# Performance work log

Hardware: AMD Instinct MI355X
Metric: run time of the kernel (lower is better)

Reference implementation:

```python
import jax, jax.numpy as jnp
import numpy as np

FOCAL_ALPHA = 0.25
FOCAL_GAMMA = 2.0
W_FOCAL = 1.0
W_DICE = 1.0
COST_MASK = 1.0
COST_DICE = 1.0
COST_CLASS = 0.0
CLS_W_MATCHED = 2.0
CLS_W_NOOBJ = 0.1


def hungarian(cost):
    """Exact Hungarian (shortest augmenting path). cost: [n, m] numpy, n <= m.
    Returns ans[i] = column assigned to row i."""
    cost = np.asarray(cost, dtype=np.float64)
    n, m = cost.shape
    assert n <= m
    INF = 1e18
    u = np.zeros(n + 1)
    v = np.zeros(m + 1)
    p = np.zeros(m + 1, dtype=np.int64)   # p[j] = row (1-indexed) matched to col j
    way = np.zeros(m + 1, dtype=np.int64)
    for i in range(1, n + 1):
        p[0] = i
        j0 = 0
        minv = np.full(m + 1, INF)
        used = np.zeros(m + 1, dtype=bool)
        while True:
            used[j0] = True
            i0 = p[j0]
            cur = cost[i0 - 1, :] - u[i0] - v[1:]
            upd = (~used[1:]) & (cur < minv[1:])
            minv[1:][upd] = cur[upd]
            way[1:][upd] = j0
            free = ~used[1:]
            j1 = int(np.argmin(np.where(free, minv[1:], INF))) + 1
            delta = minv[j1]
            u[p[used]] += delta
            v[used] -= delta
            minv[1:][free] -= delta
            j0 = j1
            if p[j0] == 0:
                break
        while j0:
            j1 = way[j0]
            p[j0] = p[j1]
            j0 = j1
    ans = np.zeros(n, dtype=np.int64)
    for j in range(1, m + 1):
        if p[j] > 0:
            ans[p[j] - 1] = j - 1
    return ans


def _focal_terms(logits):
    # sigmoid focal loss split into positive/negative per-point terms
    p = jax.nn.sigmoid(logits)
    pos = FOCAL_ALPHA * (1.0 - p) ** FOCAL_GAMMA * jax.nn.softplus(-logits)
    neg = (1.0 - FOCAL_ALPHA) * p ** FOCAL_GAMMA * jax.nn.softplus(logits)
    return pos, neg


def _inst_class_first(labels, seg, num_inst, C):
    # class of each instance = class of its FIRST point (reverse scatter so
    # earlier occurrences overwrite later ones), clamped to [0, C-1]
    inst_class = jnp.zeros((num_inst,), jnp.int32).at[labels[::-1]].set(seg[::-1])
    return jnp.clip(inst_class, 0, C - 1)


def _match_cost(pm, logits, tgt, inst_class):
    # pm [Q,N] mask logits, tgt [I,N] binary target masks
    N = pm.shape[1]
    pos, neg = _focal_terms(pm)
    c_focal = (pos @ tgt.T + neg @ (1.0 - tgt).T) / N            # [Q,I]
    p = jax.nn.sigmoid(pm)
    num = 2.0 * (p @ tgt.T)
    den = p.sum(1, keepdims=True) + tgt.sum(1)[None, :]
    c_dice = 1.0 - (num + 1.0) / (den + 1.0)                     # [Q,I]
    prob = jax.nn.softmax(logits, axis=-1)
    c_class = -prob[:, inst_class]                               # [Q,I]
    return COST_MASK * c_focal + COST_DICE * c_dice + COST_CLASS * c_class


def _batch_loss(pm, logits, labels, seg, num_inst, idx_q):
    Q, N = pm.shape
    C = logits.shape[1] - 1
    tgt = (labels[None, :] == jnp.arange(num_inst)[:, None]).astype(pm.dtype)  # [I,N]
    pm_m = pm[idx_q]                                                           # [I,N]
    # focal loss over matched (mask, target-mask) pairs
    pos, neg = _focal_terms(pm_m)
    focal = jnp.mean(pos * tgt + neg * (1.0 - tgt))
    # dice loss
    p = jax.nn.sigmoid(pm_m)
    num = 2.0 * jnp.sum(p * tgt, axis=1)
    den = jnp.sum(p, axis=1) + jnp.sum(tgt, axis=1)
    dice = jnp.mean(1.0 - (num + 1.0) / (den + 1.0))
    # classification: matched queries -> instance class, unmatched -> no-object (C)
    inst_class = _inst_class_first(labels, seg, num_inst, C)
    logp = jax.nn.log_softmax(logits, axis=-1)                 # [Q,C+1]
    ce_matched = -jnp.mean(logp[idx_q, inst_class])
    unmatched = jnp.ones((Q,), bool).at[idx_q].set(False)
    n_un = jnp.sum(unmatched)
    ce_noobj = -jnp.sum(jnp.where(unmatched, logp[:, C], 0.0)) / jnp.maximum(n_un, 1)
    cls = CLS_W_MATCHED * ce_matched + CLS_W_NOOBJ * ce_noobj
    return W_FOCAL * focal + W_DICE * dice + cls


def setup_inputs() -> dict:
    key = jax.random.key(0)
    k1, k2, k3, k4 = jax.random.split(key, 4)
    B, Q, N, I, C1 = 2, 100, 200000, 64, 6
    pred_masks = jax.random.normal(k1, (B, Q, N), dtype=jnp.float32)
    pred_logits = jax.random.normal(k2, (B, Q, C1), dtype=jnp.float32)
    labels = jax.random.randint(k3, (B, N), 0, I).astype(jnp.int32)
    # guarantee every instance id appears at least once
    labels = labels.at[:, :I].set(jnp.arange(I, dtype=jnp.int32)[None, :])
    seg = jax.random.randint(k4, (B, N), 0, C1 - 1).astype(jnp.int32)
    return {"pred_masks": pred_masks, "pred_logits": pred_logits,
            "labels": labels, "seg": seg, "num_instances": I}


def reference(pred_masks, pred_logits, labels, seg, num_instances):
    B = pred_masks.shape[0]
    C = pred_logits.shape[2] - 1
    losses = []
    for b in range(B):  # small fixed batch of events with ragged semantics
        pm, lg, lb, sg = pred_masks[b], pred_logits[b], labels[b], seg[b]
        tgt = (lb[None, :] == jnp.arange(num_instances)[:, None]).astype(pm.dtype)
        inst_class = _inst_class_first(lb, sg, num_instances, C)
        cost = _match_cost(pm, lg, tgt, inst_class)              # [Q,I]
        idx_q = jnp.asarray(hungarian(np.asarray(jax.lax.stop_gradient(cost)).T),
                            dtype=jnp.int32)                     # [I]
        losses.append(_batch_loss(pm, lg, lb, sg, num_instances, idx_q))
    return jnp.mean(jnp.stack(losses))
```

## Files before the change

kernel.cpp:

```cpp
#include <hip/hip_runtime.h>
#include <cstdint>
#include <cstddef>

constexpr int kB  = 2;
constexpr int kQ  = 100;
constexpr int kN  = 200000;
constexpr int kI  = 64;
constexpr int kC1 = 6;
constexpr int kQP = 128;

__global__ void prep_kernel(const int* __restrict__ labels,
                            int* __restrict__ cnt, int* __restrict__ firstIdx) {
  const int b = blockIdx.y;
  const int tid = threadIdx.x;
  __shared__ int lcnt[kI], lmin[kI];
  if (tid < kI) { lcnt[tid] = 0; lmin[tid] = 0x7FFFFFFF; }
  __syncthreads();
  for (int n = blockIdx.x * blockDim.x + tid; n < kN; n += gridDim.x * blockDim.x) {
    int l = labels[(size_t)b * kN + n] & (kI - 1);
    atomicAdd(&lcnt[l], 1);
    atomicMin(&lmin[l], n);
  }
  __syncthreads();
  if (tid < kI) {
    if (lcnt[tid]) atomicAdd(&cnt[b * kI + tid], lcnt[tid]);
    atomicMin(&firstIdx[b * kI + tid], lmin[tid]);
  }
}

__global__ __launch_bounds__(1024) void bucket_kernel(
    const float* __restrict__ pm, const int* __restrict__ labels,
    const int* __restrict__ cnt,
    float* __restrict__ fS, float* __restrict__ pS,
    float* __restrict__ negTot, float* __restrict__ pTot,
    float* __restrict__ costT) {
  const int q = blockIdx.x, b = blockIdx.y;
  const int tid = threadIdx.x;
  const int w = tid >> 6;
  constexpr float kScale = 16384.0f;
  constexpr double kInv  = 1.0 / 16384.0;

  __shared__ unsigned long long lS[16][kI];
  ((unsigned long long*)lS)[tid] = 0ull;
  __syncthreads();

  const float4* row4 = (const float4*)(pm + ((size_t)(b * kQ + q)) * kN);
  const int4*   lab4 = (const int4*)(labels + (size_t)b * kN);
  float negAcc = 0.f;
  constexpr int NV4 = kN / 4;

  for (int it = tid; it < NV4; it += 1024) {
    float4 xv = row4[it];
    int4   lv = lab4[it];
#define PROC(x_, l_) do {                                   \
      float x = (x_); int l = (l_) & (kI - 1);              \
      float xc = fminf(fmaxf(x, -60.f), 60.f);              \
      float t  = __expf(-xc);                               \
      float r  = 1.0f / (1.0f + t);         \
      float L  = __logf(1.0f + t);        \
      float omp = t * r;                         \
      float pos = 0.25f * omp * omp * L;                    \
      float neg = 0.75f * r * r * (L + x);                  \
      int fi = __float2int_rn((pos - neg) * kScale);        \
      int pi = __float2int_rn(r * kScale);                  \
      unsigned long long pk =                               \
        (unsigned long long)(((long long)fi) << 32) +       \
        (unsigned long long)(unsigned int)pi;               \
      atomicAdd(&lS[w][l], pk);                             \
      negAcc += neg;                                        \
    } while (0)
    PROC(xv.x, lv.x); PROC(xv.y, lv.y); PROC(xv.z, lv.z); PROC(xv.w, lv.w);
#undef PROC
  }
  __syncthreads();

  __shared__ float ffS[kI], fpS[kI];
  if (tid < kI) {
    long long fsum = 0, psum = 0;
    for (int ww = 0; ww < 16; ++ww) {
      unsigned long long s = lS[ww][tid];
      fsum += (int)(s >> 32);
      psum += (long long)(s & 0xFFFFFFFFull);
    }
    ffS[tid] = (float)((double)fsum * kInv);
    fpS[tid] = (float)((double)psum * kInv);
  }
  for (int off = 32; off; off >>= 1) negAcc += __shfl_down(negAcc, off);
  __shared__ float wsum[16];
  if ((tid & 63) == 0) wsum[w] = negAcc;
  __syncthreads();
  __shared__ float s_negTot, s_pTot;
  if (tid == 0) {
    float s = 0.f;
    for (int ww = 0; ww < 16; ++ww) s += wsum[ww];
    s_negTot = s;
  }
  if (tid < kI) {
    float vv = fpS[tid];
    for (int off = 32; off; off >>= 1) vv += __shfl_down(vv, off);
    if (tid == 0) s_pTot = vv;
  }
  __syncthreads();

  if (tid < kI) {
    float f = ffS[tid], pp = fpS[tid];
    int bq = b * kQ + q;
    fS[(size_t)bq * kI + tid] = f;
    pS[(size_t)bq * kI + tid] = pp;
    float cf = (f + s_negTot) * (1.0f / kN);
    float cd = 1.0f - (2.0f * pp + 1.0f) / (s_pTot + (float)cnt[b * kI + tid] + 1.0f);
    costT[(size_t)(b * kI + tid) * kQ + q] = cf + cd;
    if (tid == 0) { negTot[bq] = s_negTot; pTot[bq] = s_pTot; }
  }
}

template<int CTRL>
__device__ __forceinline__ int dpp_mov(int x) {
  return __builtin_amdgcn_update_dpp(x, x, CTRL, 0xF, 0xF, false);
}
template<int CTRL>
__device__ __forceinline__ float dpp_minf(float a) {
  int o = dpp_mov<CTRL>(__float_as_int(a));
  return fminf(a, __int_as_float(o));
}
__device__ __forceinline__ double rl64(double x, int l) {
  int lo = __builtin_amdgcn_readlane(__double2loint(x), l);
  int hi = __builtin_amdgcn_readlane(__double2hiint(x), l);
  return __hiloint2double(hi, lo);
}
__device__ __forceinline__ float rlf(float x, int l) {
  return __int_as_float(__builtin_amdgcn_readlane(__float_as_int(x), l));
}
__device__ __forceinline__ float packF(float v, int cid) {
  int bb = __float_as_int(v);
  bb = (bb & ~0x7F) | cid;
  return __int_as_float(bb);
}
__device__ __forceinline__ float maskF(float v) {
  return __int_as_float(__float_as_int(v) & ~0x7F);
}
__device__ __forceinline__ void comb2f(float& m1, float& m2, float o1, float o2) {
  float lo = fminf(m1, o1);
  float hi = fmaxf(m1, o1);
  m2 = fminf(hi, fminf(m2, o2));
  m1 = lo;
}
template<int CTRL>
__device__ __forceinline__ void dpp_comb2f(float& m1, float& m2) {
  float o1 = __int_as_float(dpp_mov<CTRL>(__float_as_int(m1)));
  float o2 = __int_as_float(dpp_mov<CTRL>(__float_as_int(m2)));
  comb2f(m1, m2, o1, o2);
}

__global__ void hungarian_kernel(const float* __restrict__ costT,
                                 int* __restrict__ idx_q) {
  const int b = blockIdx.x;
  const int lane = threadIdx.x;
  __shared__ float costL[kI * kQP];
  for (int t = lane; t < kI * kQP; t += 64) {
    int row = t >> 7, col = t & (kQP - 1);
    costL[t] = (col < kQ) ? costT[(size_t)b * kI * kQ + row * kQ + col] : 1e30f;
  }
  __syncthreads();

  const double INF = 1e18;
  double v0 = 0.0, v1 = 0.0;
  int p0 = 0, p1 = 0;

  double m = INF; int jm = 0;
  for (int k = 0; k < kQ; ++k) {
    double c = (double)costL[lane * kQP + k];
    if (c < m) { m = c; jm = k; }
  }
  double u_r = m;
  unsigned long long rowM = 0ull;
  for (int r = 0; r < kI; ++r) {
    int jmr = __builtin_amdgcn_readlane(jm, r);
    int curp = (jmr < 64) ? __builtin_amdgcn_readlane(p0, jmr)
                          : __builtin_amdgcn_readlane(p1, jmr - 64);
    if (curp == 0) {
      bool m0 = (jmr < 64) && (lane == jmr);
      bool m1b = (jmr >= 64) && (lane == jmr - 64);
      p0 = m0 ? r + 1 : p0;
      p1 = m1b ? r + 1 : p1;
      rowM |= 1ull << r;
    }
  }

  unsigned long long pool = ~rowM;
  unsigned long long leftover = 0ull;
  for (int pass = 0; pass < 2; ++pass) {
    unsigned long long next = 0ull;
    unsigned long long cur = pool;
    while (cur) {
      int i = __builtin_ctzll(cur) + 1;
      cur &= cur - 1;
      const float* crow = &costL[(i - 1) * kQP];
      double e0 = (double)crow[lane] - v0;
      double e1 = (double)crow[lane + 64] - v1;
      float pf0 = packF((float)e0, lane);
      float pf1 = packF((float)e1, lane + 64);
      float m1 = fminf(pf0, pf1), m2 = fmaxf(pf0, pf1);
      dpp_comb2f<0xB1>(m1, m2);
      dpp_comb2f<0x4E>(m1, m2);
      dpp_comb2f<0x141>(m1, m2);
      dpp_comb2f<0x140>(m1, m2);
      float a1 = rlf(m1, 0),  a2 = rlf(m2, 0);
      { float b1 = rlf(m1, 16), b2 = rlf(m2, 16); comb2f(a1, a2, b1, b2); }
      { float b1 = rlf(m1, 32), b2 = rlf(m2, 32); comb2f(a1, a2, b1, b2); }
      { float b1 = rlf(m1, 48), b2 = rlf(m2, 48); comb2f(a1, a2, b1, b2); }
      int cid1 = __builtin_amdgcn_readfirstlane(__float_as_int(a1) & 0x7F);
      int cid2 = __builtin_amdgcn_readfirstlane(__float_as_int(a2) & 0x7F);
      int L1 = cid1 & 63; bool sW = cid1 >= 64;
      int L2 = cid2 & 63; bool sW2 = cid2 >= 64;
      double min1 = sW  ? rl64(e1, L1) : rl64(e0, L1);
      double min2 = sW2 ? rl64(e1, L2) : rl64(e0, L2);
      double dv = min2 - min1;
      u_r = (lane == i - 1) ? min2 : u_r;
      int i0 = sW ? __builtin_amdgcn_readlane(p1, L1)
                  : __builtin_amdgcn_readlane(p0, L1);
      bool mine0 = (!sW) && (lane == L1);
      bool mine1 = sW && (lane == L1);
      p0 = mine0 ? i : p0;  v0 -= mine0 ? dv : 0.0;
      p1 = mine1 ? i : p1;  v1 -= mine1 ? dv : 0.0;
      if (i0 != 0) {
        if (pass == 0) next |= 1ull << (i0 - 1);
        else           leftover |= 1ull << (i0 - 1);
      }
    }
    pool = next;
  }
  leftover |= pool;

  const float SENT = packF(1e30f, 127);
  float u_f  = (float)u_r;
  float v0f  = (float)v0;
  float v1f  = (float)v1;
  for (int i = 1; i <= kI; ++i) {
    if (!((leftover >> (i - 1)) & 1ull)) continue;
    float minv0 = SENT, minv1 = SENT;
    int way0 = 0, way1 = 0;
    bool used0 = false, used1 = false;
    bool onpath = (lane == i - 1);
    int j0 = 0, j1 = 0;
    float c0 = costL[(i - 1) * kQP + lane];
    float c1 = costL[(i - 1) * kQP + lane + 64];
    float ui0 = rlf(u_f, i - 1);
    for (int guard = 0; guard < 2 * kQ; ++guard) {
      float pk0 = packF(c0 - ui0 - v0f, lane);
      bool up0 = (!used0) && (pk0 < minv0);
      minv0 = up0 ? pk0 : minv0;
      way0  = up0 ? j0 : way0;
      float pk1 = packF(c1 - ui0 - v1f, lane + 64);
      bool up1 = (!used1) && (pk1 < minv1);
      minv1 = up1 ? pk1 : minv1;
      way1  = up1 ? j0 : way1;
      float bm = fminf(minv0, minv1);
      bm = dpp_minf<0xB1>(bm);
      bm = dpp_minf<0x4E>(bm);
      bm = dpp_minf<0x141>(bm);
      bm = dpp_minf<0x140>(bm);
      float g = fminf(fminf(rlf(bm, 0), rlf(bm, 16)),
                      fminf(rlf(bm, 32), rlf(bm, 48)));
      int gi = __builtin_amdgcn_readfirstlane(__float_as_int(g));
      int cid = gi & 0x7F;
      float delta = __int_as_float(gi & ~0x7F);
      const int  L = cid & 63;
      const bool s = cid >= 64;
      int r1 = s ? __builtin_amdgcn_readlane(p1, L)
                 : __builtin_amdgcn_readlane(p0, L);
      int i0n = (r1 > 0) ? r1 : 1;
      float c0n = costL[(i0n - 1) * kQP + lane];
      float c1n = costL[(i0n - 1) * kQP + lane + 64];

      u_f += onpath ? delta : 0.f;
      v0f -= used0 ? delta : 0.f;
      v1f -= used1 ? delta : 0.f;
      minv0 = used0 ? minv0 : packF(maskF(minv0) - delta, lane);
      minv1 = used1 ? minv1 : packF(maskF(minv1) - delta, lane + 64);
      bool w0 = (!s) && (lane == L);
      bool w1 = s && (lane == L);
      used0 = used0 || w0;
      used1 = used1 || w1;
      minv0 = w0 ? SENT : minv0;
      minv1 = w1 ? SENT : minv1;
      j1 = cid + 1;

      if (r1 == 0) break;
      onpath = onpath || (lane == r1 - 1);
      ui0 = rlf(u_f, r1 - 1);
      j0 = j1;
      c0 = c0n;
      c1 = c1n;
    }
    int jc = j1;
    while (jc) {
      int jw = (jc <= 64) ? __builtin_amdgcn_readlane(way0, jc - 1)
                          : __builtin_amdgcn_readlane(way1, jc - 65);
      int pw;
      if (jw == 0)       pw = i;
      else if (jw <= 64) pw = __builtin_amdgcn_readlane(p0, jw - 1);
      else               pw = __builtin_amdgcn_readlane(p1, jw - 65);
      bool w0 = (jc <= 64) && (lane == jc - 1);
      bool w1 = (jc > 64) && (lane == jc - 65);
      p0 = w0 ? pw : p0;
      p1 = w1 ? pw : p1;
      jc = jw;
    }
  }
  if (p0 > 0) idx_q[b * kI + (p0 - 1)] = lane;
  if (lane < kQ - 64 && p1 > 0) idx_q[b * kI + (p1 - 1)] = lane + 64;
}

__device__ __forceinline__ float reduce128(float v, float* scratch, int tid) {
  for (int off = 32; off; off >>= 1) v += __shfl_down(v, off);
  __syncthreads();
  if ((tid & 63) == 0) scratch[tid >> 6] = v;
  __syncthreads();
  return scratch[0] + scratch[1];
}

__global__ void loss_kernel(const float* __restrict__ logits, const int* __restrict__ seg,
                            const float* __restrict__ fS, const float* __restrict__ pS,
                            const float* __restrict__ negTot, const float* __restrict__ pTot,
                            const int* __restrict__ cnt, const int* __restrict__ firstIdx,
                            const int* __restrict__ idx_q, float* __restrict__ out) {
  const int tid = threadIdx.x;
  __shared__ float lse[kQ];
  __shared__ int matched[kQ];
  __shared__ float scratch[2];
  float total = 0.f;
  for (int b = 0; b < kB; ++b) {
    if (tid < kQ) {
      const float* lr = logits + (size_t)(b * kQ + tid) * kC1;
      float m = lr[0];
#pragma unroll
      for (int c = 1; c < kC1; ++c) m = fmaxf(m, lr[c]);
      float s = 0.f;
#pragma unroll
      for (int c = 0; c < kC1; ++c) s += __expf(lr[c] - m);
      lse[tid] = m + __logf(s);
      matched[tid] = 0;
    }
    __syncthreads();
    if (tid < kI) matched[idx_q[b * kI + tid]] = 1;
    __syncthreads();

    float fo = 0.f, di = 0.f, cm = 0.f, no = 0.f, nu = 0.f;
    if (tid < kI) {
      int qi = idx_q[b * kI + tid];
      int bq = b * kQ + qi;
      float f = fS[(size_t)bq * kI + tid];
      fo = f + negTot[bq];
      float pp = pS[(size_t)bq * kI + tid];
      di = 1.f - (2.f * pp + 1.f) / (pTot[bq] + (float)cnt[b * kI + tid] + 1.f);
      int fi = firstIdx[b * kI + tid];
      fi = fi < kN ? fi : kN - 1;
      int ci = seg[(size_t)b * kN + fi];
      ci = ci < 0 ? 0 : (ci > kC1 - 2 ? kC1 - 2 : ci);
      cm = logits[(size_t)bq * kC1 + ci] - lse[qi];
    }
    if (tid < kQ && !matched[tid]) {
      no = logits[(size_t)(b * kQ + tid) * kC1 + (kC1 - 1)] - lse[tid];
      nu = 1.f;
    }
    float foS = reduce128(fo, scratch, tid);
    float diS = reduce128(di, scratch, tid);
    float cmS = reduce128(cm, scratch, tid);
    float noS = reduce128(no, scratch, tid);
    float nuS = reduce128(nu, scratch, tid);

    float focal = foS / ((float)kI * (float)kN);
    float dice  = diS / (float)kI;
    float cem   = -cmS / (float)kI;
    float cen   = -noS / fmaxf(nuS, 1.f);
    total += focal + dice + 2.0f * cem + 0.1f * cen;
    __syncthreads();
  }
  if (tid == 0) out[0] = total * (1.0f / kB);
}

extern "C" void kernel_launch(void* const* d_in, const int* in_sizes, int n_in,
                              void* d_out, int out_size, void* d_ws, size_t ws_size,
                              hipStream_t stream) {
  const float* pm     = (const float*)d_in[0];
  const float* logits = (const float*)d_in[1];
  const int*   labels = (const int*)d_in[2];
  const int*   seg    = (const int*)d_in[3];

  char* w = (char*)d_ws;
  float* fS       = (float*)w; w += (size_t)kB * kQ * kI * 4;
  float* pS       = (float*)w; w += (size_t)kB * kQ * kI * 4;
  float* negTot   = (float*)w; w += (size_t)kB * kQ * 4;
  float* pTot     = (float*)w; w += (size_t)kB * kQ * 4;
  float* costT    = (float*)w; w += (size_t)kB * kI * kQ * 4;
  int*   cnt      = (int*)w;   w += (size_t)kB * kI * 4;
  int*   firstIdx = (int*)w;   w += (size_t)kB * kI * 4;
  int*   idx_q    = (int*)w;   w += (size_t)kB * kI * 4;

  (void)hipMemsetAsync(cnt, 0, (size_t)kB * kI * 4, stream);
  (void)hipMemsetAsync(firstIdx, 0x7F, (size_t)kB * kI * 4, stream);

  prep_kernel<<<dim3(32, kB), 256, 0, stream>>>(labels, cnt, firstIdx);
  bucket_kernel<<<dim3(kQ, kB), 1024, 0, stream>>>(pm, labels, cnt, fS, pS,
                                                   negTot, pTot, costT);
  hungarian_kernel<<<kB, 64, 0, stream>>>(costT, idx_q);
  loss_kernel<<<1, 128, 0, stream>>>(logits, seg, fS, pS, negTot, pTot,
                                     cnt, firstIdx, idx_q, (float*)d_out);
}
```

Baseline: 371.8 us.

## Drop memsets via per-block partials; interleave Hungarian columns and parallelize initial greedy assignment

```diff
diff --git a/kernel.cpp b/kernel.cpp
--- a/kernel.cpp
+++ b/kernel.cpp
@@ -8,9 +8,10 @@
 constexpr int kI  = 64;
 constexpr int kC1 = 6;
 constexpr int kQP = 128;
+constexpr int kPB = 32;
 
 __global__ void prep_kernel(const int* __restrict__ labels,
-                            int* __restrict__ cnt, int* __restrict__ firstIdx) {
+                            int* __restrict__ cntPart, int* __restrict__ fiPart) {
   const int b = blockIdx.y;
   const int tid = threadIdx.x;
   __shared__ int lcnt[kI], lmin[kI];
@@ -23,14 +24,15 @@
   }
   __syncthreads();
   if (tid < kI) {
-    if (lcnt[tid]) atomicAdd(&cnt[b * kI + tid], lcnt[tid]);
-    atomicMin(&firstIdx[b * kI + tid], lmin[tid]);
+    int o = (b * kPB + blockIdx.x) * kI + tid;
+    cntPart[o] = lcnt[tid];
+    fiPart[o]  = lmin[tid];
   }
 }
 
 __global__ __launch_bounds__(1024) void bucket_kernel(
     const float* __restrict__ pm, const int* __restrict__ labels,
-    const int* __restrict__ cnt,
+    const int* __restrict__ cntPart,
     float* __restrict__ fS, float* __restrict__ pS,
     float* __restrict__ negTot, float* __restrict__ pTot,
     float* __restrict__ costT) {
@@ -103,12 +105,15 @@
   __syncthreads();
 
   if (tid < kI) {
+    int cv = 0;
+    for (int blk = 0; blk < kPB; ++blk)
+      cv += cntPart[(b * kPB + blk) * kI + tid];
     float f = ffS[tid], pp = fpS[tid];
     int bq = b * kQ + q;
     fS[(size_t)bq * kI + tid] = f;
     pS[(size_t)bq * kI + tid] = pp;
     float cf = (f + s_negTot) * (1.0f / kN);
-    float cd = 1.0f - (2.0f * pp + 1.0f) / (s_pTot + (float)cnt[b * kI + tid] + 1.0f);
+    float cd = 1.0f - (2.0f * pp + 1.0f) / (s_pTot + (float)cv + 1.0f);
     costT[(size_t)(b * kI + tid) * kQ + q] = cf + cd;
     if (tid == 0) { negTot[bq] = s_negTot; pTot[bq] = s_pTot; }
   }
@@ -157,34 +162,40 @@
   const int b = blockIdx.x;
   const int lane = threadIdx.x;
   __shared__ float costL[kI * kQP];
+  __shared__ int claim[kQP];
   for (int t = lane; t < kI * kQP; t += 64) {
     int row = t >> 7, col = t & (kQP - 1);
     costL[t] = (col < kQ) ? costT[(size_t)b * kI * kQ + row * kQ + col] : 1e30f;
   }
-  __syncthreads();
-
-  const double INF = 1e18;
+  claim[lane] = 127;
+  claim[lane + 64] = 127;
+  __syncthreads();
+
+  const int col0 = 2 * lane, col1 = 2 * lane + 1;
   double v0 = 0.0, v1 = 0.0;
   int p0 = 0, p1 = 0;
 
-  double m = INF; int jm = 0;
-  for (int k = 0; k < kQ; ++k) {
-    double c = (double)costL[lane * kQP + k];
-    if (c < m) { m = c; jm = k; }
+  double m = 1e18; int jm = 0;
+  {
+    const float4* r4 = (const float4*)&costL[lane * kQP];
+    for (int k4 = 0; k4 < kQ / 4; ++k4) {
+      float4 c = r4[k4];
+      int k = 4 * k4;
+      if ((double)c.x < m) { m = (double)c.x; jm = k; }
+      if ((double)c.y < m) { m = (double)c.y; jm = k + 1; }
+      if ((double)c.z < m) { m = (double)c.z; jm = k + 2; }
+      if ((double)c.w < m) { m = (double)c.w; jm = k + 3; }
+    }
   }
   double u_r = m;
-  unsigned long long rowM = 0ull;
-  for (int r = 0; r < kI; ++r) {
-    int jmr = __builtin_amdgcn_readlane(jm, r);
-    int curp = (jmr < 64) ? __builtin_amdgcn_readlane(p0, jmr)
-                          : __builtin_amdgcn_readlane(p1, jmr - 64);
-    if (curp == 0) {
-      bool m0 = (jmr < 64) && (lane == jmr);
-      bool m1b = (jmr >= 64) && (lane == jmr - 64);
-      p0 = m0 ? r + 1 : p0;
-      p1 = m1b ? r + 1 : p1;
-      rowM |= 1ull << r;
-    }
+
+  atomicMin(&claim[jm], lane);
+  __syncthreads();
+  unsigned long long rowM = __ballot(claim[jm] == lane);
+  {
+    int w0 = claim[col0], w1 = claim[col1];
+    p0 = (w0 < 64) ? w0 + 1 : 0;
+    p1 = (w1 < 64) ? w1 + 1 : 0;
   }
 
   unsigned long long pool = ~rowM;
@@ -195,11 +206,11 @@
     while (cur) {
       int i = __builtin_ctzll(cur) + 1;
       cur &= cur - 1;
-      const float* crow = &costL[(i - 1) * kQP];
-      double e0 = (double)crow[lane] - v0;
-      double e1 = (double)crow[lane + 64] - v1;
-      float pf0 = packF((float)e0, lane);
-      float pf1 = packF((float)e1, lane + 64);
+      float2 cc = *(const float2*)&costL[(i - 1) * kQP + col0];
+      double e0 = (double)cc.x - v0;
+      double e1 = (double)cc.y - v1;
+      float pf0 = packF((float)e0, col0);
+      float pf1 = packF((float)e1, col1);
       float m1 = fminf(pf0, pf1), m2 = fmaxf(pf0, pf1);
       dpp_comb2f<0xB1>(m1, m2);
       dpp_comb2f<0x4E>(m1, m2);
@@ -211,8 +222,8 @@
       { float b1 = rlf(m1, 48), b2 = rlf(m2, 48); comb2f(a1, a2, b1, b2); }
       int cid1 = __builtin_amdgcn_readfirstlane(__float_as_int(a1) & 0x7F);
       int cid2 = __builtin_amdgcn_readfirstlane(__float_as_int(a2) & 0x7F);
-      int L1 = cid1 & 63; bool sW = cid1 >= 64;
-      int L2 = cid2 & 63; bool sW2 = cid2 >= 64;
+      int L1 = cid1 >> 1; bool sW = cid1 & 1;
+      int L2 = cid2 >> 1; bool sW2 = cid2 & 1;
       double min1 = sW  ? rl64(e1, L1) : rl64(e0, L1);
       double min2 = sW2 ? rl64(e1, L2) : rl64(e0, L2);
       double dv = min2 - min1;
@@ -243,15 +254,15 @@
     bool used0 = false, used1 = false;
     bool onpath = (lane == i - 1);
     int j0 = 0, j1 = 0;
-    float c0 = costL[(i - 1) * kQP + lane];
-    float c1 = costL[(i - 1) * kQP + lane + 64];
+    float2 cc = *(const float2*)&costL[(i - 1) * kQP + col0];
+    float c0 = cc.x, c1 = cc.y;
     float ui0 = rlf(u_f, i - 1);
     for (int guard = 0; guard < 2 * kQ; ++guard) {
-      float pk0 = packF(c0 - ui0 - v0f, lane);
+      float pk0 = packF(c0 - ui0 - v0f, col0);
       bool up0 = (!used0) && (pk0 < minv0);
       minv0 = up0 ? pk0 : minv0;
       way0  = up0 ? j0 : way0;
-      float pk1 = packF(c1 - ui0 - v1f, lane + 64);
+      float pk1 = packF(c1 - ui0 - v1f, col1);
       bool up1 = (!used1) && (pk1 < minv1);
       minv1 = up1 ? pk1 : minv1;
       way1  = up1 ? j0 : way1;
@@ -265,19 +276,18 @@
       int gi = __builtin_amdgcn_readfirstlane(__float_as_int(g));
       int cid = gi & 0x7F;
       float delta = __int_as_float(gi & ~0x7F);
-      const int  L = cid & 63;
-      const bool s = cid >= 64;
+      const int  L = cid >> 1;
+      const bool s = cid & 1;
       int r1 = s ? __builtin_amdgcn_readlane(p1, L)
                  : __builtin_amdgcn_readlane(p0, L);
       int i0n = (r1 > 0) ? r1 : 1;
-      float c0n = costL[(i0n - 1) * kQP + lane];
-      float c1n = costL[(i0n - 1) * kQP + lane + 64];
+      float2 cn = *(const float2*)&costL[(i0n - 1) * kQP + col0];
 
       u_f += onpath ? delta : 0.f;
       v0f -= used0 ? delta : 0.f;
       v1f -= used1 ? delta : 0.f;
-      minv0 = used0 ? minv0 : packF(maskF(minv0) - delta, lane);
-      minv1 = used1 ? minv1 : packF(maskF(minv1) - delta, lane + 64);
+      minv0 = used0 ? minv0 : packF(maskF(minv0) - delta, col0);
+      minv1 = used1 ? minv1 : packF(maskF(minv1) - delta, col1);
       bool w0 = (!s) && (lane == L);
       bool w1 = s && (lane == L);
       used0 = used0 || w0;
@@ -290,26 +300,30 @@
       onpath = onpath || (lane == r1 - 1);
       ui0 = rlf(u_f, r1 - 1);
       j0 = j1;
-      c0 = c0n;
-      c1 = c1n;
+      c0 = cn.x;
+      c1 = cn.y;
     }
     int jc = j1;
     while (jc) {
-      int jw = (jc <= 64) ? __builtin_amdgcn_readlane(way0, jc - 1)
-                          : __builtin_amdgcn_readlane(way1, jc - 65);
+      int Lc = (jc - 1) >> 1, sc = (jc - 1) & 1;
+      int jw = sc ? __builtin_amdgcn_readlane(way1, Lc)
+                  : __builtin_amdgcn_readlane(way0, Lc);
       int pw;
-      if (jw == 0)       pw = i;
-      else if (jw <= 64) pw = __builtin_amdgcn_readlane(p0, jw - 1);
-      else               pw = __builtin_amdgcn_readlane(p1, jw - 65);
-      bool w0 = (jc <= 64) && (lane == jc - 1);
-      bool w1 = (jc > 64) && (lane == jc - 65);
+      if (jw == 0) pw = i;
+      else {
+        int Lw = (jw - 1) >> 1, sw = (jw - 1) & 1;
+        pw = sw ? __builtin_amdgcn_readlane(p1, Lw)
+                : __builtin_amdgcn_readlane(p0, Lw);
+      }
+      bool w0 = (!sc) && (lane == Lc);
+      bool w1 = sc && (lane == Lc);
       p0 = w0 ? pw : p0;
       p1 = w1 ? pw : p1;
       jc = jw;
     }
   }
-  if (p0 > 0) idx_q[b * kI + (p0 - 1)] = lane;
-  if (lane < kQ - 64 && p1 > 0) idx_q[b * kI + (p1 - 1)] = lane + 64;
+  if (col0 < kQ && p0 > 0) idx_q[b * kI + (p0 - 1)] = col0;
+  if (col1 < kQ && p1 > 0) idx_q[b * kI + (p1 - 1)] = col1;
 }
 
 __device__ __forceinline__ float reduce128(float v, float* scratch, int tid) {
@@ -323,7 +337,7 @@
 __global__ void loss_kernel(const float* __restrict__ logits, const int* __restrict__ seg,
                             const float* __restrict__ fS, const float* __restrict__ pS,
                             const float* __restrict__ negTot, const float* __restrict__ pTot,
-                            const int* __restrict__ cnt, const int* __restrict__ firstIdx,
+                            const int* __restrict__ cntPart, const int* __restrict__ fiPart,
                             const int* __restrict__ idx_q, float* __restrict__ out) {
   const int tid = threadIdx.x;
   __shared__ float lse[kQ];
@@ -348,13 +362,18 @@
 
     float fo = 0.f, di = 0.f, cm = 0.f, no = 0.f, nu = 0.f;
     if (tid < kI) {
+      int cv = 0, fi = 0x7FFFFFFF;
+      for (int blk = 0; blk < kPB; ++blk) {
+        int o = (b * kPB + blk) * kI + tid;
+        cv += cntPart[o];
+        fi = min(fi, fiPart[o]);
+      }
       int qi = idx_q[b * kI + tid];
       int bq = b * kQ + qi;
       float f = fS[(size_t)bq * kI + tid];
       fo = f + negTot[bq];
       float pp = pS[(size_t)bq * kI + tid];
-      di = 1.f - (2.f * pp + 1.f) / (pTot[bq] + (float)cnt[b * kI + tid] + 1.f);
-      int fi = firstIdx[b * kI + tid];
+      di = 1.f - (2.f * pp + 1.f) / (pTot[bq] + (float)cv + 1.f);
       fi = fi < kN ? fi : kN - 1;
       int ci = seg[(size_t)b * kN + fi];
       ci = ci < 0 ? 0 : (ci > kC1 - 2 ? kC1 - 2 : ci);
@@ -394,17 +413,14 @@
   float* negTot   = (float*)w; w += (size_t)kB * kQ * 4;
   float* pTot     = (float*)w; w += (size_t)kB * kQ * 4;
   float* costT    = (float*)w; w += (size_t)kB * kI * kQ * 4;
-  int*   cnt      = (int*)w;   w += (size_t)kB * kI * 4;
-  int*   firstIdx = (int*)w;   w += (size_t)kB * kI * 4;
+  int*   cntPart  = (int*)w;   w += (size_t)kB * kPB * kI * 4;
+  int*   fiPart   = (int*)w;   w += (size_t)kB * kPB * kI * 4;
   int*   idx_q    = (int*)w;   w += (size_t)kB * kI * 4;
 
-  (void)hipMemsetAsync(cnt, 0, (size_t)kB * kI * 4, stream);
-  (void)hipMemsetAsync(firstIdx, 0x7F, (size_t)kB * kI * 4, stream);
-
-  prep_kernel<<<dim3(32, kB), 256, 0, stream>>>(labels, cnt, firstIdx);
-  bucket_kernel<<<dim3(kQ, kB), 1024, 0, stream>>>(pm, labels, cnt, fS, pS,
+  prep_kernel<<<dim3(kPB, kB), 256, 0, stream>>>(labels, cntPart, fiPart);
+  bucket_kernel<<<dim3(kQ, kB), 1024, 0, stream>>>(pm, labels, cntPart, fS, pS,
                                                    negTot, pTot, costT);
   hungarian_kernel<<<kB, 64, 0, stream>>>(costT, idx_q);
   loss_kernel<<<1, 128, 0, stream>>>(logits, seg, fS, pS, negTot, pTot,
-                                     cnt, firstIdx, idx_q, (float*)d_out);
-}
+                                     cntPart, fiPart, idx_q, (float*)d_out);
+}
```

Result: faster. 355.7 us, median of 2 (-4.3%).
